# Kernel tuning notes

Hardware: AMD Instinct MI355X
Metric: run time of the kernel (lower is better)

The kernel has to match this reference:

```python
import jax, jax.numpy as jnp
import numpy as np

B, S, D = 16, 1024, 768
H = 12
HD = D // H  # 64


def setup_inputs() -> dict:
    key = jax.random.key(0)
    k1, k2, k3 = jax.random.split(key, 3)
    scale_in = 1.0 / np.sqrt(D)
    return {
        "x": jax.random.normal(k1, (B, S, D), dtype=jnp.float32),
        "w_qkv": jax.random.normal(k2, (3 * D, D), dtype=jnp.float32) * scale_in,
        "b_qkv": jnp.zeros((3 * D,), dtype=jnp.float32),
        "w_proj": jax.random.normal(k3, (D, D), dtype=jnp.float32) * scale_in,
        "b_proj": jnp.zeros((D,), dtype=jnp.float32),
    }


def reference(x, w_qkv, b_qkv, w_proj, b_proj):
    b, s, d = x.shape
    scale = HD ** -0.5
    # qkv projection: [B,S,3D] -> [3,B,H,S,HD]
    qkv = x @ w_qkv.T + b_qkv
    qkv = qkv.reshape(b, s, 3, H, HD).transpose(2, 0, 3, 1, 4)
    q, k, v = qkv[0], qkv[1], qkv[2]
    q = q * scale
    attn = jnp.einsum("bhqd,bhkd->bhqk", q, k)  # [B,H,S,S]
    attn = jax.nn.softmax(attn, axis=-1)
    # attn_dropout is identity in eval mode
    z = jnp.einsum("bhqk,bhkd->bhqd", attn, v)
    z = z.transpose(0, 2, 1, 3).reshape(b, s, d)
    return z @ w_proj.T + b_proj
```

## Files before the change

kernel.cpp:

```cpp
#include <hip/hip_runtime.h>
#include <hip/hip_bf16.h>
#include <cstdint>
#include <cstddef>

typedef __attribute__((ext_vector_type(8))) short short8;
typedef __attribute__((ext_vector_type(4))) float floatx4;
typedef __attribute__((ext_vector_type(16))) float floatx16;
typedef unsigned short u16;

__device__ __forceinline__ u16 f2bf(float f) {
  unsigned u = __float_as_uint(f);
  u += 0x7FFFu + ((u >> 16) & 1u);
  return (u16)(u >> 16);
}

__device__ __forceinline__ unsigned cvt_pk_bf16(float a, float b) {
  unsigned r;
  asm("v_cvt_pk_bf16_f32 %0, %1, %2" : "=v"(r) : "v"(a), "v"(b));
  return r;
}

__device__ __forceinline__ float fexp2(float x) {
#if __has_builtin(__builtin_amdgcn_exp2f)
  return __builtin_amdgcn_exp2f(x);
#else
  float r;
  asm("v_exp_f32 %0, %1\n\ts_nop 1" : "=v"(r) : "v"(x));
  return r;
#endif
}

__device__ __forceinline__ float frcp(float x) {
#if __has_builtin(__builtin_amdgcn_rcpf)
  return __builtin_amdgcn_rcpf(x);
#else
  float r;
  asm("v_rcp_f32 %0, %1\n\ts_nop 1" : "=v"(r) : "v"(x));
  return r;
#endif
}

__device__ __forceinline__ void gload16(const u16* g, u16* l) {
  __builtin_amdgcn_global_load_lds(
      (const __attribute__((address_space(1))) void*)g,
      (__attribute__((address_space(3))) void*)l, 16, 0, 0);
}

__global__ void cvt3_kernel(const float* __restrict__ a, u16* __restrict__ oa, int na4,
                            const float* __restrict__ b, u16* __restrict__ ob, int nb4,
                            const float* __restrict__ c, u16* __restrict__ oc, int nc4) {
  int i = blockIdx.x * blockDim.x + threadIdx.x;
  int stride = gridDim.x * blockDim.x;
  int ntot = na4 + nb4 + nc4;
  for (int idx = i; idx < ntot; idx += stride) {
    const float* src; u16* dst; int j = idx;
    if (j < na4)            { src = a; dst = oa; }
    else if (j < na4 + nb4) { src = b; dst = ob; j -= na4; }
    else                    { src = c; dst = oc; j -= na4 + nb4; }
    float4 v = reinterpret_cast<const float4*>(src)[j];
    ushort4 o = make_ushort4(f2bf(v.x), f2bf(v.y), f2bf(v.z), f2bf(v.w));
    reinterpret_cast<ushort4*>(dst)[j] = o;
  }
}

template<bool OUTF32>
__global__ __launch_bounds__(512, 2) void gemm_bt256(
    const u16* __restrict__ A, const u16* __restrict__ B,
    const float* __restrict__ bias, void* __restrict__ Cout,
    int M, int N, int K, int qcols, float qscale)
{
  __shared__ u16 As[2 * 256 * 32];
  __shared__ u16 Bs[2 * 256 * 32];
  const int tid = threadIdx.x;
  const int lane = tid & 63, w = tid >> 6;
  const int l15 = lane & 15, lhi = lane >> 4;
  const int wm = w >> 2, wn = w & 3;

  const int mblocks = M >> 8;
  const int nb = N >> 8;
  const int bid = blockIdx.x;
  const int xcd = bid & 7;
  const int local = bid >> 3;
  const int mpx = mblocks >> 3;
  const int m0 = (xcd * mpx + local / nb) << 8;
  const int n0 = (local % nb) << 8;

  const int srow = tid >> 2;
  const int scol = (tid & 3) * 8;
  const u16* aptr = A + (size_t)(m0 + srow) * K + scol;
  const u16* bptr = B + (size_t)(n0 + srow) * K + scol;
  const size_t r128 = (size_t)128 * K;

  const int ksteps = K >> 5;
  const int wbase = w * 512;

  floatx4 acc[8][4] = {};

  gload16(aptr,        As + wbase);
  gload16(aptr + r128, As + 4096 + wbase);
  gload16(bptr,        Bs + wbase);
  gload16(bptr + r128, Bs + 4096 + wbase);
  asm volatile("s_waitcnt vmcnt(0)" ::: "memory");
  __builtin_amdgcn_s_barrier();
  __builtin_amdgcn_sched_barrier(0);

  const int rowA = wm * 128 + l15;
  const int rowB = wn * 64 + l15;
  const int kof = lhi * 8;

  int cur = 0;
  for (int t = 0; t < ksteps; ++t) {
    const int nxt = cur ^ 1;
    if (t + 1 < ksteps) {
      const int k1 = (t + 1) << 5;
      gload16(aptr + k1,        As + nxt * 8192 + wbase);
      gload16(aptr + k1 + r128, As + nxt * 8192 + 4096 + wbase);
      gload16(bptr + k1,        Bs + nxt * 8192 + wbase);
      gload16(bptr + k1 + r128, Bs + nxt * 8192 + 4096 + wbase);
    }

    const u16* Ab = As + cur * 8192;
    const u16* Bb = Bs + cur * 8192;
    short8 af[8], bf[4];
#pragma unroll
    for (int i = 0; i < 8; ++i)
      af[i] = *reinterpret_cast<const short8*>(&Ab[(rowA + i * 16) * 32 + kof]);
#pragma unroll
    for (int j = 0; j < 4; ++j)
      bf[j] = *reinterpret_cast<const short8*>(&Bb[(rowB + j * 16) * 32 + kof]);

    __builtin_amdgcn_s_setprio(1);
#pragma unroll
    for (int i = 0; i < 8; ++i)
#pragma unroll
      for (int j = 0; j < 4; ++j)
        acc[i][j] = __builtin_amdgcn_mfma_f32_16x16x32_bf16(af[i], bf[j], acc[i][j], 0, 0, 0);
    __builtin_amdgcn_s_setprio(0);

    if (t + 1 < ksteps) {
      asm volatile("s_waitcnt vmcnt(0)" ::: "memory");
      __builtin_amdgcn_s_barrier();
      __builtin_amdgcn_sched_barrier(0);
    }
    cur = nxt;
  }

#pragma unroll
  for (int i = 0; i < 8; ++i)
#pragma unroll
    for (int j = 0; j < 4; ++j) {
      int row = m0 + wm * 128 + i * 16 + lhi * 4;
      int col = n0 + wn * 64 + j * 16 + l15;
      float bv = bias[col];
      float sc = (col < qcols) ? qscale : 1.0f;
#pragma unroll
      for (int r = 0; r < 4; ++r) {
        float v = (acc[i][j][r] + bv) * sc;
        if (OUTF32) reinterpret_cast<float*>(Cout)[(size_t)(row + r) * N + col] = v;
        else        reinterpret_cast<u16*>(Cout)[(size_t)(row + r) * N + col] = f2bf(v);
      }
    }
}

__global__ __launch_bounds__(256) void vtrans_kernel(
    const u16* __restrict__ qkv, u16* __restrict__ vt)
{
  __shared__ u16 T[64][72];
  const int idx = blockIdx.x;
  const int st = idx & 15;
  const int bh = idx >> 4;
  const int b = bh / 12, h = bh % 12;
  const int t = threadIdx.x;
  const int r2 = t >> 3, c8 = (t & 7) * 8;

  const u16* src = qkv + ((size_t)(b * 1024 + st * 64)) * 2304 + 1536 + h * 64;
#pragma unroll
  for (int rr = 0; rr < 2; ++rr) {
    int s = rr * 32 + r2;
    short8 v = *reinterpret_cast<const short8*>(src + (size_t)s * 2304 + c8);
    *reinterpret_cast<short8*>(&T[s][c8]) = v;
  }
  __syncthreads();
  u16* dst = vt + (size_t)bh * 64 * 1024 + st * 64;
#pragma unroll
  for (int rr = 0; rr < 2; ++rr) {
    int d = rr * 32 + r2;
    short8 o;
#pragma unroll
    for (int j = 0; j < 8; ++j) o[j] = T[c8 + j][d];
    *reinterpret_cast<short8*>(dst + (size_t)d * 1024 + c8) = o;
  }
}

__global__ __launch_bounds__(512) void attn8_kernel(
    const u16* __restrict__ qkv, const u16* __restrict__ vt, u16* __restrict__ z)
{
  constexpr int LDK = 72;
  __shared__ u16 Ks[64 * LDK];
  __shared__ u16 Vs[64 * LDK];

  const int tid = threadIdx.x;
  const int lane = tid & 63, w = tid >> 6;
  const int l31 = lane & 31, hi = lane >> 5;

  const int idx = blockIdx.x;
  const int head = idx % 192;
  const int qt   = idx / 192;
  const int b = head / 12, h = head % 12;

  const size_t rowbase = (size_t)b * 1024;
  const u16* Qp  = qkv + rowbase * 2304 + h * 64;
  const u16* Kp  = Qp + 768;
  const u16* Vtp = vt + (size_t)head * 64 * 1024;

  const int q0 = qt * 256 + w * 32;

  short8 qf[4];
#pragma unroll
  for (int c = 0; c < 4; ++c)
    qf[c] = *reinterpret_cast<const short8*>(
        Qp + (size_t)(q0 + l31) * 2304 + c * 16 + hi * 8);

  union { unsigned u[4]; short8 v; } ONE;
#pragma unroll
  for (int i = 0; i < 4; ++i) ONE.u[i] = 0x3F803F80u;
  const short8 ones = ONE.v;

  const int srow = tid >> 3, scol = (tid & 7) * 8;

  const u16* kstage = Kp + (size_t)srow * 2304 + scol;
  const u16* vstage = Vtp + (size_t)srow * 1024 + scol;
  constexpr size_t KADV = (size_t)64 * 2304;
  constexpr size_t VADV = 64;

  u16* const ksw = &Ks[srow * LDK + scol];
  u16* const vsw = &Vs[srow * LDK + scol];
  const u16* const ks0 = &Ks[l31 * LDK + hi * 8];
  const u16* const ks1 = ks0 + 32 * LDK;
  const u16* const vs0 = &Vs[l31 * LDK + hi * 8];
  const u16* const vs1 = vs0 + 32 * LDK;

  short8 kvr = *reinterpret_cast<const short8*>(kstage);
  short8 vvr = *reinterpret_cast<const short8*>(vstage);
  kstage += KADV; vstage += VADV;

  floatx16 oacc0 = {}, oacc1 = {}, lacc = {};

  for (int kt = 0; kt < 16; ++kt) {
    __syncthreads();
    *reinterpret_cast<short8*>(ksw) = kvr;
    *reinterpret_cast<short8*>(vsw) = vvr;
    __syncthreads();

    if (kt < 15) {
      kvr = *reinterpret_cast<const short8*>(kstage);
      vvr = *reinterpret_cast<const short8*>(vstage);
      kstage += KADV; vstage += VADV;
    }

    floatx16 s0 = {}, s1 = {};
    __builtin_amdgcn_s_setprio(1);
#pragma unroll
    for (int c = 0; c < 4; ++c) {
      short8 kf0 = *reinterpret_cast<const short8*>(ks0 + c * 16);
      short8 kf1 = *reinterpret_cast<const short8*>(ks1 + c * 16);
      s0 = __builtin_amdgcn_mfma_f32_32x32x16_bf16(kf0, qf[c], s0, 0, 0, 0);
      s1 = __builtin_amdgcn_mfma_f32_32x32x16_bf16(kf1, qf[c], s1, 0, 0, 0);
    }
    __builtin_amdgcn_s_setprio(0);

#pragma unroll
    for (int r = 0; r < 16; ++r) {
      s0[r] = fexp2(s0[r]);
      s1[r] = fexp2(s1[r]);
    }

    short8 pa[4];
#pragma unroll
    for (int c = 0; c < 4; ++c) {
      const floatx16& sv = (c >> 1) ? s1 : s0;
      const int B0 = (c & 1) * 8, B1 = B0 + 4;
      unsigned x0 = cvt_pk_bf16(sv[B0],     sv[B0 + 1]);
      unsigned x1 = cvt_pk_bf16(sv[B0 + 2], sv[B0 + 3]);
      unsigned y0 = cvt_pk_bf16(sv[B1],     sv[B1 + 1]);
      unsigned y1 = cvt_pk_bf16(sv[B1 + 2], sv[B1 + 3]);
      asm("s_nop 1\n\tv_permlane32_swap_b32 %0, %1" : "+v"(x0), "+v"(y0));
      asm("s_nop 1\n\tv_permlane32_swap_b32 %0, %1" : "+v"(x1), "+v"(y1));
      union { unsigned u[4]; short8 v; } P;
      P.u[0] = x0; P.u[1] = x1; P.u[2] = y0; P.u[3] = y1;
      pa[c] = P.v;
    }

    __builtin_amdgcn_s_setprio(1);
#pragma unroll
    for (int c = 0; c < 4; ++c) {
      short8 vf0 = *reinterpret_cast<const short8*>(vs0 + c * 16);
      short8 vf1 = *reinterpret_cast<const short8*>(vs1 + c * 16);
      oacc0 = __builtin_amdgcn_mfma_f32_32x32x16_bf16(pa[c], vf0, oacc0, 0, 0, 0);
      oacc1 = __builtin_amdgcn_mfma_f32_32x32x16_bf16(pa[c], vf1, oacc1, 0, 0, 0);
      lacc  = __builtin_amdgcn_mfma_f32_32x32x16_bf16(pa[c], ones, lacc, 0, 0, 0);
    }
    __builtin_amdgcn_s_setprio(0);
  }

#pragma unroll
  for (int r = 0; r < 16; ++r) {
    int q = (r & 3) + 8 * (r >> 2) + 4 * hi;
    float li = frcp(lacc[r]);
    size_t orow = (rowbase + q0 + q) * (size_t)768 + h * 64;
    z[orow + l31]      = f2bf(oacc0[r] * li);
    z[orow + 32 + l31] = f2bf(oacc1[r] * li);
  }
}

extern "C" void kernel_launch(void* const* d_in, const int* in_sizes, int n_in,
                              void* d_out, int out_size, void* d_ws, size_t ws_size,
                              hipStream_t stream) {
  (void)in_sizes; (void)n_in; (void)out_size; (void)ws_size;
  const float* x      = (const float*)d_in[0];
  const float* w_qkv  = (const float*)d_in[1];
  const float* b_qkv  = (const float*)d_in[2];
  const float* w_proj = (const float*)d_in[3];
  const float* b_proj = (const float*)d_in[4];
  float* out = (float*)d_out;

  const int BS = 16 * 1024;
  const int D = 768, N3 = 2304;
  const float QSC = 0.180336880f;

  u16* xb  = (u16*)d_ws;
  u16* wqb = xb  + (size_t)BS * D;
  u16* wpb = wqb + (size_t)N3 * D;
  u16* qkv = wpb + (size_t)D * D;
  u16* zb  = qkv + (size_t)BS * N3;
  u16* vtb = xb;

  cvt3_kernel<<<2048, 256, 0, stream>>>(x, xb, BS * D / 4,
                                        w_qkv, wqb, N3 * D / 4,
                                        w_proj, wpb, D * D / 4);

  gemm_bt256<false><<<(BS / 256) * (N3 / 256), 512, 0, stream>>>(
      xb, wqb, b_qkv, qkv, BS, N3, D, 768, QSC);
  vtrans_kernel<<<192 * 16, 256, 0, stream>>>(qkv, vtb);
  attn8_kernel<<<192 * 4, 512, 0, stream>>>(qkv, vtb, zb);
  gemm_bt256<true><<<(BS / 256) * (D / 256), 512, 0, stream>>>(
      zb, wpb, b_proj, out, BS, D, D, 0, 1.0f);
}
```

Measured before the change: 233.6 us.

## Triple-buffer GEMM with interleaved phase barriers; double-buffer attention K/V tiles

The GEMM moves from a double-buffered to a triple-buffered LDS pipeline that prefetches two K-steps ahead. Each step is split into four MFMA phases, each separated by a barrier and preceded by one staged global-to-LDS load, so memory traffic is interleaved with compute. The launch_bounds occupancy hint of 2 is dropped, and LDS use grows to 96KB per block. The attention kernel double-buffers its K/V shared tiles, which removes one __syncthreads per iteration; the extra barriers in the GEMM and the larger LDS footprint may cut occupancy.

```diff
diff --git a/kernel.cpp b/kernel.cpp
--- a/kernel.cpp
+++ b/kernel.cpp
@@ -44,6 +44,12 @@
   __builtin_amdgcn_global_load_lds(
       (const __attribute__((address_space(1))) void*)g,
       (__attribute__((address_space(3))) void*)l, 16, 0, 0);
+}
+
+__device__ __forceinline__ void phase_barrier() {
+  __builtin_amdgcn_sched_barrier(0);
+  __builtin_amdgcn_s_barrier();
+  __builtin_amdgcn_sched_barrier(0);
 }
 
 __global__ void cvt3_kernel(const float* __restrict__ a, u16* __restrict__ oa, int na4,
@@ -64,13 +70,13 @@
 }
 
 template<bool OUTF32>
-__global__ __launch_bounds__(512, 2) void gemm_bt256(
+__global__ __launch_bounds__(512) void gemm_bt256p(
     const u16* __restrict__ A, const u16* __restrict__ B,
     const float* __restrict__ bias, void* __restrict__ Cout,
     int M, int N, int K, int qcols, float qscale)
 {
-  __shared__ u16 As[2 * 256 * 32];
-  __shared__ u16 Bs[2 * 256 * 32];
+  __shared__ u16 As[3 * 8192];
+  __shared__ u16 Bs[3 * 8192];
   const int tid = threadIdx.x;
   const int lane = tid & 63, w = tid >> 6;
   const int l15 = lane & 15, lhi = lane >> 4;
@@ -90,59 +96,93 @@
   const u16* aptr = A + (size_t)(m0 + srow) * K + scol;
   const u16* bptr = B + (size_t)(n0 + srow) * K + scol;
   const size_t r128 = (size_t)128 * K;
-
+  const int wbase = w * 512;
   const int ksteps = K >> 5;
-  const int wbase = w * 512;
 
   floatx4 acc[8][4] = {};
 
-  gload16(aptr,        As + wbase);
-  gload16(aptr + r128, As + 4096 + wbase);
-  gload16(bptr,        Bs + wbase);
-  gload16(bptr + r128, Bs + 4096 + wbase);
-  asm volatile("s_waitcnt vmcnt(0)" ::: "memory");
-  __builtin_amdgcn_s_barrier();
-  __builtin_amdgcn_sched_barrier(0);
-
-  const int rowA = wm * 128 + l15;
-  const int rowB = wn * 64 + l15;
+  gload16(aptr,             As + wbase);
+  gload16(aptr + r128,      As + 4096 + wbase);
+  gload16(bptr,             Bs + wbase);
+  gload16(bptr + r128,      Bs + 4096 + wbase);
+  gload16(aptr + 32,        As + 8192 + wbase);
+  gload16(aptr + 32 + r128, As + 8192 + 4096 + wbase);
+  gload16(bptr + 32,        Bs + 8192 + wbase);
+  gload16(bptr + 32 + r128, Bs + 8192 + 4096 + wbase);
+  asm volatile("s_waitcnt vmcnt(4)" ::: "memory");
+  phase_barrier();
+
+  const int rA = wm * 128 + l15;
+  const int rB = wn * 64 + l15;
   const int kof = lhi * 8;
 
-  int cur = 0;
+  int bc = 0, bs = 2;
   for (int t = 0; t < ksteps; ++t) {
-    const int nxt = cur ^ 1;
+    const bool stage = (t + 2 < ksteps);
+    const int k2 = (t + 2) << 5;
+    const u16* Ab = As + bc * 8192;
+    const u16* Bb = Bs + bc * 8192;
+    u16* Asd = As + bs * 8192 + wbase;
+    u16* Bsd = Bs + bs * 8192 + wbase;
+    short8 af[8], bf[4];
+
+    if (stage) gload16(aptr + k2, Asd);
+#pragma unroll
+    for (int i = 0; i < 4; ++i)
+      af[i] = *reinterpret_cast<const short8*>(&Ab[(rA + i * 16) * 32 + kof]);
+    bf[0] = *reinterpret_cast<const short8*>(&Bb[(rB)      * 32 + kof]);
+    bf[1] = *reinterpret_cast<const short8*>(&Bb[(rB + 16) * 32 + kof]);
+    phase_barrier();
+    __builtin_amdgcn_s_setprio(1);
+#pragma unroll
+    for (int i = 0; i < 4; ++i) {
+      acc[i][0] = __builtin_amdgcn_mfma_f32_16x16x32_bf16(af[i], bf[0], acc[i][0], 0, 0, 0);
+      acc[i][1] = __builtin_amdgcn_mfma_f32_16x16x32_bf16(af[i], bf[1], acc[i][1], 0, 0, 0);
+    }
+    __builtin_amdgcn_s_setprio(0);
+
+    if (stage) gload16(aptr + k2 + r128, Asd + 4096);
+    bf[2] = *reinterpret_cast<const short8*>(&Bb[(rB + 32) * 32 + kof]);
+    bf[3] = *reinterpret_cast<const short8*>(&Bb[(rB + 48) * 32 + kof]);
+    phase_barrier();
+    __builtin_amdgcn_s_setprio(1);
+#pragma unroll
+    for (int i = 0; i < 4; ++i) {
+      acc[i][2] = __builtin_amdgcn_mfma_f32_16x16x32_bf16(af[i], bf[2], acc[i][2], 0, 0, 0);
+      acc[i][3] = __builtin_amdgcn_mfma_f32_16x16x32_bf16(af[i], bf[3], acc[i][3], 0, 0, 0);
+    }
+    __builtin_amdgcn_s_setprio(0);
+
+    if (stage) gload16(bptr + k2, Bsd);
+#pragma unroll
+    for (int i = 0; i < 4; ++i)
+      af[4 + i] = *reinterpret_cast<const short8*>(&Ab[(rA + 64 + i * 16) * 32 + kof]);
+    phase_barrier();
+    __builtin_amdgcn_s_setprio(1);
+#pragma unroll
+    for (int i = 0; i < 4; ++i) {
+      acc[4 + i][0] = __builtin_amdgcn_mfma_f32_16x16x32_bf16(af[4 + i], bf[0], acc[4 + i][0], 0, 0, 0);
+      acc[4 + i][1] = __builtin_amdgcn_mfma_f32_16x16x32_bf16(af[4 + i], bf[1], acc[4 + i][1], 0, 0, 0);
+    }
+    __builtin_amdgcn_s_setprio(0);
+
+    if (stage) gload16(bptr + k2 + r128, Bsd + 4096);
+    phase_barrier();
+    __builtin_amdgcn_s_setprio(1);
+#pragma unroll
+    for (int i = 0; i < 4; ++i) {
+      acc[4 + i][2] = __builtin_amdgcn_mfma_f32_16x16x32_bf16(af[4 + i], bf[2], acc[4 + i][2], 0, 0, 0);
+      acc[4 + i][3] = __builtin_amdgcn_mfma_f32_16x16x32_bf16(af[4 + i], bf[3], acc[4 + i][3], 0, 0, 0);
+    }
+    __builtin_amdgcn_s_setprio(0);
+
     if (t + 1 < ksteps) {
-      const int k1 = (t + 1) << 5;
-      gload16(aptr + k1,        As + nxt * 8192 + wbase);
-      gload16(aptr + k1 + r128, As + nxt * 8192 + 4096 + wbase);
-      gload16(bptr + k1,        Bs + nxt * 8192 + wbase);
-      gload16(bptr + k1 + r128, Bs + nxt * 8192 + 4096 + wbase);
-    }
-
-    const u16* Ab = As + cur * 8192;
-    const u16* Bb = Bs + cur * 8192;
-    short8 af[8], bf[4];
-#pragma unroll
-    for (int i = 0; i < 8; ++i)
-      af[i] = *reinterpret_cast<const short8*>(&Ab[(rowA + i * 16) * 32 + kof]);
-#pragma unroll
-    for (int j = 0; j < 4; ++j)
-      bf[j] = *reinterpret_cast<const short8*>(&Bb[(rowB + j * 16) * 32 + kof]);
-
-    __builtin_amdgcn_s_setprio(1);
-#pragma unroll
-    for (int i = 0; i < 8; ++i)
-#pragma unroll
-      for (int j = 0; j < 4; ++j)
-        acc[i][j] = __builtin_amdgcn_mfma_f32_16x16x32_bf16(af[i], bf[j], acc[i][j], 0, 0, 0);
-    __builtin_amdgcn_s_setprio(0);
-
-    if (t + 1 < ksteps) {
-      asm volatile("s_waitcnt vmcnt(0)" ::: "memory");
-      __builtin_amdgcn_s_barrier();
-      __builtin_amdgcn_sched_barrier(0);
-    }
-    cur = nxt;
+      if (stage) asm volatile("s_waitcnt vmcnt(4)" ::: "memory");
+      else       asm volatile("s_waitcnt vmcnt(0)" ::: "memory");
+      phase_barrier();
+    }
+    bc = (bc == 2) ? 0 : bc + 1;
+    bs = (bs == 2) ? 0 : bs + 1;
   }
 
 #pragma unroll
@@ -192,12 +232,13 @@
   }
 }
 
-__global__ __launch_bounds__(512) void attn8_kernel(
+__global__ __launch_bounds__(512) void attn9_kernel(
     const u16* __restrict__ qkv, const u16* __restrict__ vt, u16* __restrict__ z)
 {
   constexpr int LDK = 72;
-  __shared__ u16 Ks[64 * LDK];
-  __shared__ u16 Vs[64 * LDK];
+  constexpr int SLOT = 64 * LDK;
+  __shared__ u16 Ks[2 * SLOT];
+  __shared__ u16 Vs[2 * SLOT];
 
   const int tid = threadIdx.x;
   const int lane = tid & 63, w = tid >> 6;
@@ -236,9 +277,7 @@
   u16* const ksw = &Ks[srow * LDK + scol];
   u16* const vsw = &Vs[srow * LDK + scol];
   const u16* const ks0 = &Ks[l31 * LDK + hi * 8];
-  const u16* const ks1 = ks0 + 32 * LDK;
   const u16* const vs0 = &Vs[l31 * LDK + hi * 8];
-  const u16* const vs1 = vs0 + 32 * LDK;
 
   short8 kvr = *reinterpret_cast<const short8*>(kstage);
   short8 vvr = *reinterpret_cast<const short8*>(vstage);
@@ -247,9 +286,9 @@
   floatx16 oacc0 = {}, oacc1 = {}, lacc = {};
 
   for (int kt = 0; kt < 16; ++kt) {
-    __syncthreads();
-    *reinterpret_cast<short8*>(ksw) = kvr;
-    *reinterpret_cast<short8*>(vsw) = vvr;
+    const int so = (kt & 1) * SLOT;
+    *reinterpret_cast<short8*>(ksw + so) = kvr;
+    *reinterpret_cast<short8*>(vsw + so) = vvr;
     __syncthreads();
 
     if (kt < 15) {
@@ -258,12 +297,15 @@
       kstage += KADV; vstage += VADV;
     }
 
+    const u16* ka = ks0 + so;
+    const u16* va = vs0 + so;
+
     floatx16 s0 = {}, s1 = {};
     __builtin_amdgcn_s_setprio(1);
 #pragma unroll
     for (int c = 0; c < 4; ++c) {
-      short8 kf0 = *reinterpret_cast<const short8*>(ks0 + c * 16);
-      short8 kf1 = *reinterpret_cast<const short8*>(ks1 + c * 16);
+      short8 kf0 = *reinterpret_cast<const short8*>(ka + c * 16);
+      short8 kf1 = *reinterpret_cast<const short8*>(ka + 32 * LDK + c * 16);
       s0 = __builtin_amdgcn_mfma_f32_32x32x16_bf16(kf0, qf[c], s0, 0, 0, 0);
       s1 = __builtin_amdgcn_mfma_f32_32x32x16_bf16(kf1, qf[c], s1, 0, 0, 0);
     }
@@ -294,8 +336,8 @@
     __builtin_amdgcn_s_setprio(1);
 #pragma unroll
     for (int c = 0; c < 4; ++c) {
-      short8 vf0 = *reinterpret_cast<const short8*>(vs0 + c * 16);
-      short8 vf1 = *reinterpret_cast<const short8*>(vs1 + c * 16);
+      short8 vf0 = *reinterpret_cast<const short8*>(va + c * 16);
+      short8 vf1 = *reinterpret_cast<const short8*>(va + 32 * LDK + c * 16);
       oacc0 = __builtin_amdgcn_mfma_f32_32x32x16_bf16(pa[c], vf0, oacc0, 0, 0, 0);
       oacc1 = __builtin_amdgcn_mfma_f32_32x32x16_bf16(pa[c], vf1, oacc1, 0, 0, 0);
       lacc  = __builtin_amdgcn_mfma_f32_32x32x16_bf16(pa[c], ones, lacc, 0, 0, 0);
@@ -339,10 +381,10 @@
                                         w_qkv, wqb, N3 * D / 4,
                                         w_proj, wpb, D * D / 4);
 
-  gemm_bt256<false><<<(BS / 256) * (N3 / 256), 512, 0, stream>>>(
+  gemm_bt256p<false><<<(BS / 256) * (N3 / 256), 512, 0, stream>>>(
       xb, wqb, b_qkv, qkv, BS, N3, D, 768, QSC);
   vtrans_kernel<<<192 * 16, 256, 0, stream>>>(qkv, vtb);
-  attn8_kernel<<<192 * 4, 512, 0, stream>>>(qkv, vtb, zb);
-  gemm_bt256<true><<<(BS / 256) * (D / 256), 512, 0, stream>>>(
+  attn9_kernel<<<192 * 4, 512, 0, stream>>>(qkv, vtb, zb);
+  gemm_bt256p<true><<<(BS / 256) * (D / 256), 512, 0, stream>>>(
       zb, wpb, b_proj, out, BS, D, D, 0, 1.0f);
 }
```

Result: slower. 244.8 us (+4.8%).
